# Kernel optimization log

Measured on AMD Instinct MI355X. Metric: run time of the kernel, lower is better.

## Reference

```python
import jax, jax.numpy as jnp
import numpy as np

N_NODES = 50000
N_EDGES = 800000
D_IN, D_HID, D_OUT = 128, 128, 64


def setup_inputs() -> dict:
    key = jax.random.key(0)
    ks = jax.random.split(key, 10)
    return {
        "x": jax.random.normal(ks[0], (N_NODES, D_IN), dtype=jnp.float32),
        "edge_row": jax.random.randint(ks[1], (N_EDGES,), 0, N_NODES, dtype=jnp.int32),
        "edge_col": jax.random.randint(ks[2], (N_EDGES,), 0, N_NODES, dtype=jnp.int32),
        "edge_val": jax.random.uniform(ks[3], (N_EDGES,), dtype=jnp.float32),
        "W1": jax.random.normal(ks[4], (D_IN, D_HID), dtype=jnp.float32) * (1.0 / np.sqrt(D_HID)),
        "b1": jax.random.normal(ks[5], (D_HID,), dtype=jnp.float32) * (1.0 / np.sqrt(D_HID)),
        "W2": jax.random.normal(ks[6], (D_HID, D_HID), dtype=jnp.float32) * (1.0 / np.sqrt(D_HID)),
        "b2": jax.random.normal(ks[7], (D_HID,), dtype=jnp.float32) * (1.0 / np.sqrt(D_HID)),
        "W3": jax.random.normal(ks[8], (D_HID, D_OUT), dtype=jnp.float32) * (1.0 / np.sqrt(D_OUT)),
        "b3": jax.random.normal(ks[9], (D_OUT,), dtype=jnp.float32) * (1.0 / np.sqrt(D_OUT)),
    }


def _gcn_layer(x, edge_row, edge_col, edge_val, W, b):
    # support = x @ W          : dense GEMM [N, d_out]
    support = x @ W
    # spmm(adj, support)[i] = sum_e with row[e]==i: val[e] * support[col[e]]
    gathered = support[edge_col] * edge_val[:, None]  # [E, d_out]
    agg = jax.ops.segment_sum(gathered, edge_row, num_segments=x.shape[0])
    return agg + b


def reference(x, edge_row, edge_col, edge_val, W1, b1, W2, b2, W3, b3):
    # Layer 1 + ReLU (dropout is identity in eval)
    h = jax.nn.relu(_gcn_layer(x, edge_row, edge_col, edge_val, W1, b1))
    # Layer 2 + ReLU
    h = jax.nn.relu(_gcn_layer(h, edge_row, edge_col, edge_val, W2, b2))
    # Layer 3 (no activation)
    return _gcn_layer(h, edge_row, edge_col, edge_val, W3, b3)
```

## Files before the change

### kernel.cpp

```cpp
#include <hip/hip_runtime.h>

#define N_NODES 50000
#define N_EDGES 800000
#define SCAN_TILE 2048
#define CNT_STRIDE 16
#define GEMM_BLOCKS 256

static_assert(N_NODES < 65536, "col must fit in 16 bits for packed CSR");

typedef __attribute__((ext_vector_type(4))) float f32x4;
typedef __attribute__((ext_vector_type(8))) short bf16x8;

__device__ inline unsigned short f32_to_bf16(float f) {
    unsigned int u = __builtin_bit_cast(unsigned int, f);
    u += 0x7FFF + ((u >> 16) & 1);
    return (unsigned short)(u >> 16);
}
__device__ inline float bf16_to_f32(unsigned short h) {
    unsigned int u = ((unsigned int)h) << 16;
    return __builtin_bit_cast(float, u);
}

#define W128  (128 * 128)
#define W64   (128 * 64)
#define CNT4  (N_NODES * CNT_STRIDE / 4)

__global__ void prep(const float* __restrict__ W1, const float* __restrict__ W2,
                     const float* __restrict__ W3, unsigned short* __restrict__ Wt1,
                     unsigned short* __restrict__ Wt2, unsigned short* __restrict__ Wt3,
                     int* __restrict__ cnt) {
    long long gid = (long long)blockIdx.x * blockDim.x + threadIdx.x;
    long long r = gid;
    if (r < W128) {
        int k = (int)r / 128, m = (int)r % 128;
        Wt1[m * 128 + k] = f32_to_bf16(W1[r]);
        return;
    }
    r -= W128;
    if (r < W128) {
        int k = (int)r / 128, m = (int)r % 128;
        Wt2[m * 128 + k] = f32_to_bf16(W2[r]);
        return;
    }
    r -= W128;
    if (r < W64) {
        int k = (int)r / 64, m = (int)r % 64;
        Wt3[m * 128 + k] = f32_to_bf16(W3[r]);
        return;
    }
    r -= W64;
    if (r < CNT4) {
        int4 z = {0, 0, 0, 0};
        reinterpret_cast<int4*>(cnt)[r] = z;
    }
}

__global__ void rank_histogram(const int* __restrict__ erow, int* __restrict__ cnt,
                               int* __restrict__ rank) {
    int e = blockIdx.x * blockDim.x + threadIdx.x;
    if (e < N_EDGES) rank[e] = atomicAdd(&cnt[(size_t)erow[e] * CNT_STRIDE], 1);
}

__global__ void scan_fused(const int* __restrict__ cnt, int* __restrict__ tsum,
                           int* __restrict__ done, int* __restrict__ rptr,
                           int n, int ntiles) {
    __shared__ int sums[256];
    __shared__ int off_s;
    const int t = threadIdx.x;
    const int b = blockIdx.x;
    const int base = b * SCAN_TILE + t * 8;
    int v[8], pref[8];
    int s = 0;
#pragma unroll
    for (int i = 0; i < 8; ++i) {
        v[i] = (base + i < n) ? cnt[(size_t)(base + i) * CNT_STRIDE] : 0;
        s += v[i];
    }
    sums[t] = s;
    __syncthreads();
    for (int off = 1; off < 256; off <<= 1) {
        int x = (t >= off) ? sums[t - off] : 0;
        __syncthreads();
        sums[t] += x;
        __syncthreads();
    }
    int run = sums[t] - s;
#pragma unroll
    for (int i = 0; i < 8; ++i) {
        pref[i] = run;
        run += v[i];
    }
    if (t == 255) {
        tsum[b] = run;
        __threadfence();
        atomicAdd(done, 1);
    }
    if (t == 0) {
        while (__hip_atomic_load(done, __ATOMIC_ACQUIRE, __HIP_MEMORY_SCOPE_AGENT) <
               ntiles) {
        }
        __threadfence();
        int off = 0;
        for (int i = 0; i < b; ++i) off += tsum[i];
        off_s = off;
        if (b == 0) {
            int tot = 0;
            for (int i = 0; i < ntiles; ++i) tot += tsum[i];
            rptr[n] = tot;
        }
    }
    __syncthreads();
    const int off = off_s;
#pragma unroll
    for (int i = 0; i < 8; ++i) {
        int idx = base + i;
        if (idx < n) rptr[idx] = pref[i] + off;
    }
}

template <int NOUT, bool OUT_BF16, bool IN_F32>
__device__ __forceinline__ void gemm_body(
    const void* __restrict__ Xin, const unsigned short* __restrict__ Wt,
    void* __restrict__ Yv, int N, int ntiles, int bid, int nblocks,
    unsigned short* Xs, unsigned short* Ws) {
    constexpr int K = 128;
    constexpr int KP = K + 8;
    constexpr int NT = NOUT / 16;

    const int tid = threadIdx.x;
    const int wave = tid >> 6;
    const int lane = tid & 63;
    const int m = lane & 15;
    const int quad = lane >> 4;
    const int rowbase = wave * 16;

    for (int idx = tid; idx < NOUT * 16; idx += 256) {
        int r = idx >> 4, ch = idx & 15;
        uint4 v = *reinterpret_cast<const uint4*>(Wt + r * K + ch * 8);
        *reinterpret_cast<uint4*>(Ws + r * KP + ch * 8) = v;
    }

    for (int tile = bid; tile < ntiles; tile += nblocks) {
        const int block_row = tile * 64;
        if (IN_F32) {
            const float* xf = (const float*)Xin;
            for (int idx = tid; idx < 64 * 16; idx += 256) {
                int r = idx >> 4, ch = idx & 15;
                int gr = block_row + r;
                if (gr >= N) gr = N - 1;
                const float4* xp =
                    reinterpret_cast<const float4*>(xf + (size_t)gr * K + ch * 8);
                float4 a = xp[0], b = xp[1];
                uint4 o;
                o.x = (unsigned int)f32_to_bf16(a.x) | ((unsigned int)f32_to_bf16(a.y) << 16);
                o.y = (unsigned int)f32_to_bf16(a.z) | ((unsigned int)f32_to_bf16(a.w) << 16);
                o.z = (unsigned int)f32_to_bf16(b.x) | ((unsigned int)f32_to_bf16(b.y) << 16);
                o.w = (unsigned int)f32_to_bf16(b.z) | ((unsigned int)f32_to_bf16(b.w) << 16);
                *reinterpret_cast<uint4*>(Xs + r * KP + ch * 8) = o;
            }
        } else {
            const unsigned short* xb = (const unsigned short*)Xin;
            for (int idx = tid; idx < 64 * 16; idx += 256) {
                int r = idx >> 4, ch = idx & 15;
                int gr = block_row + r;
                if (gr >= N) gr = N - 1;
                uint4 v = *reinterpret_cast<const uint4*>(xb + (size_t)gr * K + ch * 8);
                *reinterpret_cast<uint4*>(Xs + r * KP + ch * 8) = v;
            }
        }
        __syncthreads();

        f32x4 acc[NT];
#pragma unroll
        for (int t = 0; t < NT; ++t) acc[t] = (f32x4){0.f, 0.f, 0.f, 0.f};

#pragma unroll
        for (int kt = 0; kt < 4; ++kt) {
            bf16x8 a = *reinterpret_cast<const bf16x8*>(
                Xs + (rowbase + m) * KP + kt * 32 + quad * 8);
#pragma unroll
            for (int t = 0; t < NT; ++t) {
                bf16x8 b = *reinterpret_cast<const bf16x8*>(
                    Ws + (t * 16 + m) * KP + kt * 32 + quad * 8);
                acc[t] = __builtin_amdgcn_mfma_f32_16x16x32_bf16(a, b, acc[t], 0, 0, 0);
            }
        }
        __syncthreads();

#pragma unroll
        for (int t = 0; t < NT; ++t) {
#pragma unroll
            for (int r = 0; r < 4; ++r) {
                int grow = block_row + rowbase + quad * 4 + r;
                if (grow < N) {
                    if (OUT_BF16)
                        reinterpret_cast<unsigned short*>(Yv)[(size_t)grow * NOUT + t * 16 + m] =
                            f32_to_bf16(acc[t][r]);
                    else
                        reinterpret_cast<float*>(Yv)[(size_t)grow * NOUT + t * 16 + m] = acc[t][r];
                }
            }
        }
    }
}

template <int NOUT, bool OUT_BF16>
__global__ __launch_bounds__(256) void gemm_mfma(
    const unsigned short* __restrict__ Xb, const unsigned short* __restrict__ Wt,
    void* __restrict__ Yv, int N, int ntiles) {
    constexpr int KP = 128 + 8;
    __shared__ unsigned short Xs[64 * KP];
    __shared__ unsigned short Ws[NOUT * KP];
    gemm_body<NOUT, OUT_BF16, false>(Xb, Wt, Yv, N, ntiles, blockIdx.x, gridDim.x,
                                     Xs, Ws);
}

__global__ __launch_bounds__(256) void gemm1_fill(
    const float* __restrict__ x, const unsigned short* __restrict__ Wt,
    unsigned short* __restrict__ Yb, int N, int ntiles,
    const int* __restrict__ erow, const int* __restrict__ ecol,
    const float* __restrict__ eval, const int* __restrict__ rptr,
    const int* __restrict__ rank, unsigned int* __restrict__ cpack) {
    constexpr int KP = 128 + 8;
    __shared__ unsigned short Xs[64 * KP];
    __shared__ unsigned short Ws[128 * KP];
    if (blockIdx.x < GEMM_BLOCKS) {
        gemm_body<128, true, true>(x, Wt, Yb, N, ntiles, blockIdx.x, GEMM_BLOCKS,
                                   Xs, Ws);
    } else {
        int e = (blockIdx.x - GEMM_BLOCKS) * blockDim.x + threadIdx.x;
        if (e < N_EDGES) {
            int slot = rptr[erow[e]] + rank[e];
            unsigned int p = (unsigned int)(ecol[e] & 0xFFFF) |
                             ((unsigned int)f32_to_bf16(eval[e]) << 16);
            cpack[slot] = p;
        }
    }
}

__global__ void aggregate_bf16(const unsigned short* __restrict__ S,
                               const int* __restrict__ rptr,
                               const unsigned int* __restrict__ cpack,
                               const float* __restrict__ bias,
                               unsigned short* __restrict__ outb, int N) {
    const int node = blockIdx.x * (blockDim.x / 16) + threadIdx.x / 16;
    const int f8 = threadIdx.x & 15;
    if (node >= N) return;
    const int beg = rptr[node];
    const int end = rptr[node + 1];
    float acc[8];
#pragma unroll
    for (int i = 0; i < 8; ++i) acc[i] = bias[f8 * 8 + i];
    int j = beg;
    for (; j + 8 <= end; j += 8) {
        unsigned int p[8];
        uint4 s[8];
#pragma unroll
        for (int u = 0; u < 8; ++u) p[u] = cpack[j + u];
#pragma unroll
        for (int u = 0; u < 8; ++u)
            s[u] = *reinterpret_cast<const uint4*>(S + (size_t)(p[u] & 0xFFFF) * 128 + f8 * 8);
#pragma unroll
        for (int u = 0; u < 8; ++u) {
            const float v = bf16_to_f32((unsigned short)(p[u] >> 16));
            const unsigned short* sp = reinterpret_cast<const unsigned short*>(&s[u]);
#pragma unroll
            for (int i = 0; i < 8; ++i) acc[i] = fmaf(v, bf16_to_f32(sp[i]), acc[i]);
        }
    }
    if (j + 4 <= end) {
        unsigned int p[4];
        uint4 s[4];
#pragma unroll
        for (int u = 0; u < 4; ++u) p[u] = cpack[j + u];
#pragma unroll
        for (int u = 0; u < 4; ++u)
            s[u] = *reinterpret_cast<const uint4*>(S + (size_t)(p[u] & 0xFFFF) * 128 + f8 * 8);
#pragma unroll
        for (int u = 0; u < 4; ++u) {
            const float v = bf16_to_f32((unsigned short)(p[u] >> 16));
            const unsigned short* sp = reinterpret_cast<const unsigned short*>(&s[u]);
#pragma unroll
            for (int i = 0; i < 8; ++i) acc[i] = fmaf(v, bf16_to_f32(sp[i]), acc[i]);
        }
        j += 4;
    }
    if (j + 2 <= end) {
        unsigned int p[2];
        uint4 s[2];
#pragma unroll
        for (int u = 0; u < 2; ++u) p[u] = cpack[j + u];
#pragma unroll
        for (int u = 0; u < 2; ++u)
            s[u] = *reinterpret_cast<const uint4*>(S + (size_t)(p[u] & 0xFFFF) * 128 + f8 * 8);
#pragma unroll
        for (int u = 0; u < 2; ++u) {
            const float v = bf16_to_f32((unsigned short)(p[u] >> 16));
            const unsigned short* sp = reinterpret_cast<const unsigned short*>(&s[u]);
#pragma unroll
            for (int i = 0; i < 8; ++i) acc[i] = fmaf(v, bf16_to_f32(sp[i]), acc[i]);
        }
        j += 2;
    }
    if (j < end) {
        unsigned int p = cpack[j];
        uint4 s = *reinterpret_cast<const uint4*>(S + (size_t)(p & 0xFFFF) * 128 + f8 * 8);
        const float v = bf16_to_f32((unsigned short)(p >> 16));
        const unsigned short* sp = reinterpret_cast<const unsigned short*>(&s);
#pragma unroll
        for (int i = 0; i < 8; ++i) acc[i] = fmaf(v, bf16_to_f32(sp[i]), acc[i]);
    }
    unsigned short o[8];
#pragma unroll
    for (int i = 0; i < 8; ++i) o[i] = f32_to_bf16(fmaxf(acc[i], 0.0f));
    *reinterpret_cast<uint4*>(outb + (size_t)node * 128 + f8 * 8) =
        *reinterpret_cast<uint4*>(o);
}

__global__ void aggregate_bf16_64(const unsigned short* __restrict__ S,
                                  const int* __restrict__ rptr,
                                  const unsigned int* __restrict__ cpack,
                                  const float* __restrict__ bias,
                                  float* __restrict__ out, int N) {
    const int node = blockIdx.x * (blockDim.x / 16) + threadIdx.x / 16;
    const int f4 = threadIdx.x & 15;
    if (node >= N) return;
    const int beg = rptr[node];
    const int end = rptr[node + 1];
    float acc[4];
#pragma unroll
    for (int i = 0; i < 4; ++i) acc[i] = bias[f4 * 4 + i];
    int j = beg;
    for (; j + 8 <= end; j += 8) {
        unsigned int p[8];
        uint2 s[8];
#pragma unroll
        for (int u = 0; u < 8; ++u) p[u] = cpack[j + u];
#pragma unroll
        for (int u = 0; u < 8; ++u)
            s[u] = *reinterpret_cast<const uint2*>(S + (size_t)(p[u] & 0xFFFF) * 64 + f4 * 4);
#pragma unroll
        for (int u = 0; u < 8; ++u) {
            const float v = bf16_to_f32((unsigned short)(p[u] >> 16));
            const unsigned short* sp = reinterpret_cast<const unsigned short*>(&s[u]);
#pragma unroll
            for (int i = 0; i < 4; ++i) acc[i] = fmaf(v, bf16_to_f32(sp[i]), acc[i]);
        }
    }
    if (j + 4 <= end) {
        unsigned int p[4];
        uint2 s[4];
#pragma unroll
        for (int u = 0; u < 4; ++u) p[u] = cpack[j + u];
#pragma unroll
        for (int u = 0; u < 4; ++u)
            s[u] = *reinterpret_cast<const uint2*>(S + (size_t)(p[u] & 0xFFFF) * 64 + f4 * 4);
#pragma unroll
        for (int u = 0; u < 4; ++u) {
            const float v = bf16_to_f32((unsigned short)(p[u] >> 16));
            const unsigned short* sp = reinterpret_cast<const unsigned short*>(&s[u]);
#pragma unroll
            for (int i = 0; i < 4; ++i) acc[i] = fmaf(v, bf16_to_f32(sp[i]), acc[i]);
        }
        j += 4;
    }
    if (j + 2 <= end) {
        unsigned int p[2];
        uint2 s[2];
#pragma unroll
        for (int u = 0; u < 2; ++u) p[u] = cpack[j + u];
#pragma unroll
        for (int u = 0; u < 2; ++u)
            s[u] = *reinterpret_cast<const uint2*>(S + (size_t)(p[u] & 0xFFFF) * 64 + f4 * 4);
#pragma unroll
        for (int u = 0; u < 2; ++u) {
            const float v = bf16_to_f32((unsigned short)(p[u] >> 16));
            const unsigned short* sp = reinterpret_cast<const unsigned short*>(&s[u]);
#pragma unroll
            for (int i = 0; i < 4; ++i) acc[i] = fmaf(v, bf16_to_f32(sp[i]), acc[i]);
        }
        j += 2;
    }
    if (j < end) {
        unsigned int p = cpack[j];
        uint2 s = *reinterpret_cast<const uint2*>(S + (size_t)(p & 0xFFFF) * 64 + f4 * 4);
        const float v = bf16_to_f32((unsigned short)(p >> 16));
        const unsigned short* sp = reinterpret_cast<const unsigned short*>(&s);
#pragma unroll
        for (int i = 0; i < 4; ++i) acc[i] = fmaf(v, bf16_to_f32(sp[i]), acc[i]);
    }
    float4 o = {acc[0], acc[1], acc[2], acc[3]};
    *reinterpret_cast<float4*>(out + (size_t)node * 64 + f4 * 4) = o;
}

extern "C" void kernel_launch(void* const* d_in, const int* in_sizes, int n_in,
                              void* d_out, int out_size, void* d_ws, size_t ws_size,
                              hipStream_t stream) {
    const float* x    = (const float*)d_in[0];
    const int*   erow = (const int*)d_in[1];
    const int*   ecol = (const int*)d_in[2];
    const float* eval = (const float*)d_in[3];
    const float* W1   = (const float*)d_in[4];
    const float* b1   = (const float*)d_in[5];
    const float* W2   = (const float*)d_in[6];
    const float* b2   = (const float*)d_in[7];
    const float* W3   = (const float*)d_in[8];
    const float* b3   = (const float*)d_in[9];
    float* out = (float*)d_out;

    const size_t nf = (size_t)N_NODES * 128;
    unsigned short* Xb  = (unsigned short*)d_ws;
    unsigned short* Ab  = Xb + nf;
    unsigned short* Wt1 = Ab + nf;
    unsigned short* Wt2 = Wt1 + 128 * 128;
    unsigned short* Wt3 = Wt2 + 128 * 128;
    int*   cnt    = (int*)(Wt3 + 64 * 128);
    int*   rank   = cnt + (size_t)N_NODES * CNT_STRIDE;
    int*   rptr   = rank + N_EDGES;
    unsigned int* cpack = (unsigned int*)(rptr + N_NODES + 1);
    int*   stsum  = (int*)(cpack + N_EDGES);
    int*   done   = cnt + 1;

    const int blk = 256;
    const int ntiles_g = (N_NODES + 63) / 64;
    const int agg_grid = (int)(((long long)N_NODES * 16 + blk - 1) / blk);
    const int ntiles = (N_NODES + SCAN_TILE - 1) / SCAN_TILE;
    const int fill_blocks = (N_EDGES + blk - 1) / blk;

    {
        long long total = W128 + W128 + W64 + CNT4;
        prep<<<(int)((total + blk - 1) / blk), blk, 0, stream>>>(
            W1, W2, W3, Wt1, Wt2, Wt3, cnt);
    }
    rank_histogram<<<(N_EDGES + blk - 1) / blk, blk, 0, stream>>>(erow, cnt, rank);
    scan_fused<<<ntiles, 256, 0, stream>>>(cnt, stsum, done, rptr, N_NODES, ntiles);

    gemm1_fill<<<GEMM_BLOCKS + fill_blocks, 256, 0, stream>>>(
        x, Wt1, Ab, N_NODES, ntiles_g, erow, ecol, eval, rptr, rank, cpack);
    aggregate_bf16<<<agg_grid, blk, 0, stream>>>(Ab, rptr, cpack, b1, Xb, N_NODES);

    gemm_mfma<128, true><<<GEMM_BLOCKS, 256, 0, stream>>>(Xb, Wt2, Ab, N_NODES, ntiles_g);
    aggregate_bf16<<<agg_grid, blk, 0, stream>>>(Ab, rptr, cpack, b2, Xb, N_NODES);

    gemm_mfma<64, true><<<GEMM_BLOCKS, 256, 0, stream>>>(Xb, Wt3, Ab, N_NODES, ntiles_g);
    aggregate_bf16_64<<<agg_grid, blk, 0, stream>>>(Ab, rptr, cpack, b3, out, N_NODES);
}
```

Measured before the change: 262.8 us.

## Fuse sparse aggregation into following layer's MFMA GEMM via shared-memory tile

New measurement: 320.9 us. 22.1% more time.

```diff
diff --git a/kernel.cpp b/kernel.cpp
--- a/kernel.cpp
+++ b/kernel.cpp
@@ -5,6 +5,7 @@
 #define SCAN_TILE 2048
 #define CNT_STRIDE 16
 #define GEMM_BLOCKS 256
+#define HIST_BLOCKS ((N_EDGES + 255) / 256)
 
 static_assert(N_NODES < 65536, "col must fit in 16 bits for packed CSR");
 
@@ -25,12 +26,26 @@
 #define W64   (128 * 64)
 #define CNT4  (N_NODES * CNT_STRIDE / 4)
 
-__global__ void prep(const float* __restrict__ W1, const float* __restrict__ W2,
-                     const float* __restrict__ W3, unsigned short* __restrict__ Wt1,
-                     unsigned short* __restrict__ Wt2, unsigned short* __restrict__ Wt3,
-                     int* __restrict__ cnt) {
-    long long gid = (long long)blockIdx.x * blockDim.x + threadIdx.x;
-    long long r = gid;
+__global__ void zero_cnt(int* __restrict__ cnt) {
+    int i = blockIdx.x * blockDim.x + threadIdx.x;
+    if (i < CNT4) {
+        int4 z = {0, 0, 0, 0};
+        reinterpret_cast<int4*>(cnt)[i] = z;
+    }
+}
+
+__global__ void hist_wt(const int* __restrict__ erow, int* __restrict__ cnt,
+                        int* __restrict__ rank, const float* __restrict__ W1,
+                        const float* __restrict__ W2, const float* __restrict__ W3,
+                        unsigned short* __restrict__ Wt1,
+                        unsigned short* __restrict__ Wt2,
+                        unsigned short* __restrict__ Wt3) {
+    if (blockIdx.x < HIST_BLOCKS) {
+        int e = blockIdx.x * blockDim.x + threadIdx.x;
+        if (e < N_EDGES) rank[e] = atomicAdd(&cnt[(size_t)erow[e] * CNT_STRIDE], 1);
+        return;
+    }
+    long long r = (long long)(blockIdx.x - HIST_BLOCKS) * blockDim.x + threadIdx.x;
     if (r < W128) {
         int k = (int)r / 128, m = (int)r % 128;
         Wt1[m * 128 + k] = f32_to_bf16(W1[r]);
@@ -46,19 +61,7 @@
     if (r < W64) {
         int k = (int)r / 64, m = (int)r % 64;
         Wt3[m * 128 + k] = f32_to_bf16(W3[r]);
-        return;
-    }
-    r -= W64;
-    if (r < CNT4) {
-        int4 z = {0, 0, 0, 0};
-        reinterpret_cast<int4*>(cnt)[r] = z;
-    }
-}
-
-__global__ void rank_histogram(const int* __restrict__ erow, int* __restrict__ cnt,
-                               int* __restrict__ rank) {
-    int e = blockIdx.x * blockDim.x + threadIdx.x;
-    if (e < N_EDGES) rank[e] = atomicAdd(&cnt[(size_t)erow[e] * CNT_STRIDE], 1);
+    }
 }
 
 __global__ void scan_fused(const int* __restrict__ cnt, int* __restrict__ tsum,
@@ -118,15 +121,13 @@
     }
 }
 
-template <int NOUT, bool OUT_BF16, bool IN_F32>
-__device__ __forceinline__ void gemm_body(
-    const void* __restrict__ Xin, const unsigned short* __restrict__ Wt,
-    void* __restrict__ Yv, int N, int ntiles, int bid, int nblocks,
-    unsigned short* Xs, unsigned short* Ws) {
-    constexpr int K = 128;
-    constexpr int KP = K + 8;
+template <int NOUT>
+__device__ __forceinline__ void mfma_phase(const unsigned short* Xs,
+                                           const unsigned short* Ws,
+                                           unsigned short* __restrict__ Yb,
+                                           int block_row, int N) {
+    constexpr int KP = 128 + 8;
     constexpr int NT = NOUT / 16;
-
     const int tid = threadIdx.x;
     const int wave = tid >> 6;
     const int lane = tid & 63;
@@ -134,85 +135,31 @@
     const int quad = lane >> 4;
     const int rowbase = wave * 16;
 
-    for (int idx = tid; idx < NOUT * 16; idx += 256) {
-        int r = idx >> 4, ch = idx & 15;
-        uint4 v = *reinterpret_cast<const uint4*>(Wt + r * K + ch * 8);
-        *reinterpret_cast<uint4*>(Ws + r * KP + ch * 8) = v;
-    }
-
-    for (int tile = bid; tile < ntiles; tile += nblocks) {
-        const int block_row = tile * 64;
-        if (IN_F32) {
-            const float* xf = (const float*)Xin;
-            for (int idx = tid; idx < 64 * 16; idx += 256) {
-                int r = idx >> 4, ch = idx & 15;
-                int gr = block_row + r;
-                if (gr >= N) gr = N - 1;
-                const float4* xp =
-                    reinterpret_cast<const float4*>(xf + (size_t)gr * K + ch * 8);
-                float4 a = xp[0], b = xp[1];
-                uint4 o;
-                o.x = (unsigned int)f32_to_bf16(a.x) | ((unsigned int)f32_to_bf16(a.y) << 16);
-                o.y = (unsigned int)f32_to_bf16(a.z) | ((unsigned int)f32_to_bf16(a.w) << 16);
-                o.z = (unsigned int)f32_to_bf16(b.x) | ((unsigned int)f32_to_bf16(b.y) << 16);
-                o.w = (unsigned int)f32_to_bf16(b.z) | ((unsigned int)f32_to_bf16(b.w) << 16);
-                *reinterpret_cast<uint4*>(Xs + r * KP + ch * 8) = o;
-            }
-        } else {
-            const unsigned short* xb = (const unsigned short*)Xin;
-            for (int idx = tid; idx < 64 * 16; idx += 256) {
-                int r = idx >> 4, ch = idx & 15;
-                int gr = block_row + r;
-                if (gr >= N) gr = N - 1;
-                uint4 v = *reinterpret_cast<const uint4*>(xb + (size_t)gr * K + ch * 8);
-                *reinterpret_cast<uint4*>(Xs + r * KP + ch * 8) = v;
-            }
-        }
-        __syncthreads();
-
-        f32x4 acc[NT];
-#pragma unroll
-        for (int t = 0; t < NT; ++t) acc[t] = (f32x4){0.f, 0.f, 0.f, 0.f};
-
-#pragma unroll
-        for (int kt = 0; kt < 4; ++kt) {
-            bf16x8 a = *reinterpret_cast<const bf16x8*>(
-                Xs + (rowbase + m) * KP + kt * 32 + quad * 8);
-#pragma unroll
-            for (int t = 0; t < NT; ++t) {
-                bf16x8 b = *reinterpret_cast<const bf16x8*>(
-                    Ws + (t * 16 + m) * KP + kt * 32 + quad * 8);
-                acc[t] = __builtin_amdgcn_mfma_f32_16x16x32_bf16(a, b, acc[t], 0, 0, 0);
-            }
-        }
-        __syncthreads();
-
+    f32x4 acc[NT];
+#pragma unroll
+    for (int t = 0; t < NT; ++t) acc[t] = (f32x4){0.f, 0.f, 0.f, 0.f};
+
+#pragma unroll
+    for (int kt = 0; kt < 4; ++kt) {
+        bf16x8 a = *reinterpret_cast<const bf16x8*>(
+            Xs + (rowbase + m) * KP + kt * 32 + quad * 8);
 #pragma unroll
         for (int t = 0; t < NT; ++t) {
-#pragma unroll
-            for (int r = 0; r < 4; ++r) {
-                int grow = block_row + rowbase + quad * 4 + r;
-                if (grow < N) {
-                    if (OUT_BF16)
-                        reinterpret_cast<unsigned short*>(Yv)[(size_t)grow * NOUT + t * 16 + m] =
-                            f32_to_bf16(acc[t][r]);
-                    else
-                        reinterpret_cast<float*>(Yv)[(size_t)grow * NOUT + t * 16 + m] = acc[t][r];
-                }
-            }
-        }
-    }
-}
-
-template <int NOUT, bool OUT_BF16>
-__global__ __launch_bounds__(256) void gemm_mfma(
-    const unsigned short* __restrict__ Xb, const unsigned short* __restrict__ Wt,
-    void* __restrict__ Yv, int N, int ntiles) {
-    constexpr int KP = 128 + 8;
-    __shared__ unsigned short Xs[64 * KP];
-    __shared__ unsigned short Ws[NOUT * KP];
-    gemm_body<NOUT, OUT_BF16, false>(Xb, Wt, Yv, N, ntiles, blockIdx.x, gridDim.x,
-                                     Xs, Ws);
+            bf16x8 b = *reinterpret_cast<const bf16x8*>(
+                Ws + (t * 16 + m) * KP + kt * 32 + quad * 8);
+            acc[t] = __builtin_amdgcn_mfma_f32_16x16x32_bf16(a, b, acc[t], 0, 0, 0);
+        }
+    }
+
+#pragma unroll
+    for (int t = 0; t < NT; ++t) {
+#pragma unroll
+        for (int r = 0; r < 4; ++r) {
+            int grow = block_row + rowbase + quad * 4 + r;
+            if (grow < N)
+                Yb[(size_t)grow * NOUT + t * 16 + m] = f32_to_bf16(acc[t][r]);
+        }
+    }
 }
 
 __global__ __launch_bounds__(256) void gemm1_fill(
@@ -224,97 +171,171 @@
     constexpr int KP = 128 + 8;
     __shared__ unsigned short Xs[64 * KP];
     __shared__ unsigned short Ws[128 * KP];
-    if (blockIdx.x < GEMM_BLOCKS) {
-        gemm_body<128, true, true>(x, Wt, Yb, N, ntiles, blockIdx.x, GEMM_BLOCKS,
-                                   Xs, Ws);
-    } else {
-        int e = (blockIdx.x - GEMM_BLOCKS) * blockDim.x + threadIdx.x;
+    const int tid = threadIdx.x;
+
+    if (blockIdx.x >= GEMM_BLOCKS) {
+        int e = (blockIdx.x - GEMM_BLOCKS) * blockDim.x + tid;
         if (e < N_EDGES) {
             int slot = rptr[erow[e]] + rank[e];
             unsigned int p = (unsigned int)(ecol[e] & 0xFFFF) |
                              ((unsigned int)f32_to_bf16(eval[e]) << 16);
             cpack[slot] = p;
         }
-    }
-}
-
-__global__ void aggregate_bf16(const unsigned short* __restrict__ S,
-                               const int* __restrict__ rptr,
-                               const unsigned int* __restrict__ cpack,
-                               const float* __restrict__ bias,
-                               unsigned short* __restrict__ outb, int N) {
-    const int node = blockIdx.x * (blockDim.x / 16) + threadIdx.x / 16;
-    const int f8 = threadIdx.x & 15;
-    if (node >= N) return;
-    const int beg = rptr[node];
-    const int end = rptr[node + 1];
-    float acc[8];
-#pragma unroll
-    for (int i = 0; i < 8; ++i) acc[i] = bias[f8 * 8 + i];
-    int j = beg;
-    for (; j + 8 <= end; j += 8) {
-        unsigned int p[8];
-        uint4 s[8];
-#pragma unroll
-        for (int u = 0; u < 8; ++u) p[u] = cpack[j + u];
-#pragma unroll
-        for (int u = 0; u < 8; ++u)
-            s[u] = *reinterpret_cast<const uint4*>(S + (size_t)(p[u] & 0xFFFF) * 128 + f8 * 8);
-#pragma unroll
-        for (int u = 0; u < 8; ++u) {
-            const float v = bf16_to_f32((unsigned short)(p[u] >> 16));
-            const unsigned short* sp = reinterpret_cast<const unsigned short*>(&s[u]);
-#pragma unroll
-            for (int i = 0; i < 8; ++i) acc[i] = fmaf(v, bf16_to_f32(sp[i]), acc[i]);
-        }
-    }
-    if (j + 4 <= end) {
-        unsigned int p[4];
-        uint4 s[4];
-#pragma unroll
-        for (int u = 0; u < 4; ++u) p[u] = cpack[j + u];
-#pragma unroll
-        for (int u = 0; u < 4; ++u)
-            s[u] = *reinterpret_cast<const uint4*>(S + (size_t)(p[u] & 0xFFFF) * 128 + f8 * 8);
-#pragma unroll
-        for (int u = 0; u < 4; ++u) {
-            const float v = bf16_to_f32((unsigned short)(p[u] >> 16));
-            const unsigned short* sp = reinterpret_cast<const unsigned short*>(&s[u]);
-#pragma unroll
-            for (int i = 0; i < 8; ++i) acc[i] = fmaf(v, bf16_to_f32(sp[i]), acc[i]);
-        }
-        j += 4;
-    }
-    if (j + 2 <= end) {
-        unsigned int p[2];
-        uint4 s[2];
-#pragma unroll
-        for (int u = 0; u < 2; ++u) p[u] = cpack[j + u];
-#pragma unroll
-        for (int u = 0; u < 2; ++u)
-            s[u] = *reinterpret_cast<const uint4*>(S + (size_t)(p[u] & 0xFFFF) * 128 + f8 * 8);
-#pragma unroll
-        for (int u = 0; u < 2; ++u) {
-            const float v = bf16_to_f32((unsigned short)(p[u] >> 16));
-            const unsigned short* sp = reinterpret_cast<const unsigned short*>(&s[u]);
-#pragma unroll
-            for (int i = 0; i < 8; ++i) acc[i] = fmaf(v, bf16_to_f32(sp[i]), acc[i]);
-        }
-        j += 2;
-    }
-    if (j < end) {
-        unsigned int p = cpack[j];
-        uint4 s = *reinterpret_cast<const uint4*>(S + (size_t)(p & 0xFFFF) * 128 + f8 * 8);
-        const float v = bf16_to_f32((unsigned short)(p >> 16));
-        const unsigned short* sp = reinterpret_cast<const unsigned short*>(&s);
-#pragma unroll
-        for (int i = 0; i < 8; ++i) acc[i] = fmaf(v, bf16_to_f32(sp[i]), acc[i]);
-    }
-    unsigned short o[8];
-#pragma unroll
-    for (int i = 0; i < 8; ++i) o[i] = f32_to_bf16(fmaxf(acc[i], 0.0f));
-    *reinterpret_cast<uint4*>(outb + (size_t)node * 128 + f8 * 8) =
-        *reinterpret_cast<uint4*>(o);
+        return;
+    }
+
+    for (int idx = tid; idx < 128 * 16; idx += 256) {
+        int r = idx >> 4, ch = idx & 15;
+        uint4 v = *reinterpret_cast<const uint4*>(Wt + r * 128 + ch * 8);
+        *reinterpret_cast<uint4*>(Ws + r * KP + ch * 8) = v;
+    }
+
+    for (int tile = blockIdx.x; tile < ntiles; tile += GEMM_BLOCKS) {
+        const int block_row = tile * 64;
+        for (int idx = tid; idx < 64 * 16; idx += 256) {
+            int r = idx >> 4, ch = idx & 15;
+            int gr = block_row + r;
+            if (gr >= N) gr = N - 1;
+            const float4* xp =
+                reinterpret_cast<const float4*>(x + (size_t)gr * 128 + ch * 8);
+            float4 a = xp[0], b = xp[1];
+            uint4 o;
+            o.x = (unsigned int)f32_to_bf16(a.x) | ((unsigned int)f32_to_bf16(a.y) << 16);
+            o.y = (unsigned int)f32_to_bf16(a.z) | ((unsigned int)f32_to_bf16(a.w) << 16);
+            o.z = (unsigned int)f32_to_bf16(b.x) | ((unsigned int)f32_to_bf16(b.y) << 16);
+            o.w = (unsigned int)f32_to_bf16(b.z) | ((unsigned int)f32_to_bf16(b.w) << 16);
+            *reinterpret_cast<uint4*>(Xs + r * KP + ch * 8) = o;
+        }
+        __syncthreads();
+        mfma_phase<128>(Xs, Ws, Yb, block_row, N);
+        __syncthreads();
+    }
+}
+
+template <int NOUT>
+__global__ __launch_bounds__(256) void gemm_fused_agg(
+    const unsigned short* __restrict__ S,
+    const int* __restrict__ rptr, const unsigned int* __restrict__ cpack,
+    const float* __restrict__ bias,
+    const unsigned short* __restrict__ Wt,
+    unsigned short* __restrict__ Yb,
+    int N, int ntiles) {
+    constexpr int KP = 128 + 8;
+    __shared__ unsigned short Xs[64 * KP];
+    __shared__ unsigned short Ws[NOUT * KP];
+    const int tid = threadIdx.x;
+    const int group = tid >> 4;
+    const int f8 = tid & 15;
+
+    for (int idx = tid; idx < NOUT * 16; idx += 256) {
+        int r = idx >> 4, ch = idx & 15;
+        uint4 v = *reinterpret_cast<const uint4*>(Wt + r * 128 + ch * 8);
+        *reinterpret_cast<uint4*>(Ws + r * KP + ch * 8) = v;
+    }
+
+    float bv[8];
+#pragma unroll
+    for (int i = 0; i < 8; ++i) bv[i] = bias[f8 * 8 + i];
+
+    for (int tile = blockIdx.x; tile < ntiles; tile += gridDim.x) {
+        const int block_row = tile * 64;
+#pragma unroll
+        for (int r4 = 0; r4 < 4; ++r4) {
+            const int row = r4 * 16 + group;
+            const int node = block_row + row;
+            float acc[8];
+#pragma unroll
+            for (int i = 0; i < 8; ++i) acc[i] = bv[i];
+            if (node < N) {
+                const int beg = rptr[node];
+                const int end = rptr[node + 1];
+                int j = beg;
+                for (; j + 8 <= end; j += 8) {
+                    unsigned int p[8];
+                    uint4 s[8];
+#pragma unroll
+                    for (int u = 0; u < 8; ++u) p[u] = cpack[j + u];
+#pragma unroll
+                    for (int u = 0; u < 8; ++u)
+                        s[u] = *reinterpret_cast<const uint4*>(
+                            S + (size_t)(p[u] & 0xFFFF) * 128 + f8 * 8);
+#pragma unroll
+                    for (int u = 0; u < 8; ++u) {
+                        const float v = bf16_to_f32((unsigned short)(p[u] >> 16));
+                        const unsigned short* sp =
+                            reinterpret_cast<const unsigned short*>(&s[u]);
+#pragma unroll
+                        for (int i = 0; i < 8; ++i)
+                            acc[i] = fmaf(v, bf16_to_f32(sp[i]), acc[i]);
+                    }
+                }
+                if (j + 4 <= end) {
+                    unsigned int p[4];
+                    uint4 s[4];
+#pragma unroll
+                    for (int u = 0; u < 4; ++u) p[u] = cpack[j + u];
+#pragma unroll
+                    for (int u = 0; u < 4; ++u)
+                        s[u] = *reinterpret_cast<const uint4*>(
+                            S + (size_t)(p[u] & 0xFFFF) * 128 + f8 * 8);
+#pragma unroll
+                    for (int u = 0; u < 4; ++u) {
+                        const float v = bf16_to_f32((unsigned short)(p[u] >> 16));
+                        const unsigned short* sp =
+                            reinterpret_cast<const unsigned short*>(&s[u]);
+#pragma unroll
+                        for (int i = 0; i < 8; ++i)
+                            acc[i] = fmaf(v, bf16_to_f32(sp[i]), acc[i]);
+                    }
+                    j += 4;
+                }
+                if (j + 2 <= end) {
+                    unsigned int p[2];
+                    uint4 s[2];
+#pragma unroll
+                    for (int u = 0; u < 2; ++u) p[u] = cpack[j + u];
+#pragma unroll
+                    for (int u = 0; u < 2; ++u)
+                        s[u] = *reinterpret_cast<const uint4*>(
+                            S + (size_t)(p[u] & 0xFFFF) * 128 + f8 * 8);
+#pragma unroll
+                    for (int u = 0; u < 2; ++u) {
+                        const float v = bf16_to_f32((unsigned short)(p[u] >> 16));
+                        const unsigned short* sp =
+                            reinterpret_cast<const unsigned short*>(&s[u]);
+#pragma unroll
+                        for (int i = 0; i < 8; ++i)
+                            acc[i] = fmaf(v, bf16_to_f32(sp[i]), acc[i]);
+                    }
+                    j += 2;
+                }
+                if (j < end) {
+                    unsigned int p = cpack[j];
+                    uint4 s = *reinterpret_cast<const uint4*>(
+                        S + (size_t)(p & 0xFFFF) * 128 + f8 * 8);
+                    const float v = bf16_to_f32((unsigned short)(p >> 16));
+                    const unsigned short* sp =
+                        reinterpret_cast<const unsigned short*>(&s);
+#pragma unroll
+                    for (int i = 0; i < 8; ++i)
+                        acc[i] = fmaf(v, bf16_to_f32(sp[i]), acc[i]);
+                }
+            }
+            uint4 o;
+            o.x = (unsigned int)f32_to_bf16(fmaxf(acc[0], 0.f)) |
+                  ((unsigned int)f32_to_bf16(fmaxf(acc[1], 0.f)) << 16);
+            o.y = (unsigned int)f32_to_bf16(fmaxf(acc[2], 0.f)) |
+                  ((unsigned int)f32_to_bf16(fmaxf(acc[3], 0.f)) << 16);
+            o.z = (unsigned int)f32_to_bf16(fmaxf(acc[4], 0.f)) |
+                  ((unsigned int)f32_to_bf16(fmaxf(acc[5], 0.f)) << 16);
+            o.w = (unsigned int)f32_to_bf16(fmaxf(acc[6], 0.f)) |
+                  ((unsigned int)f32_to_bf16(fmaxf(acc[7], 0.f)) << 16);
+            *reinterpret_cast<uint4*>(Xs + row * KP + f8 * 8) = o;
+        }
+        __syncthreads();
+        mfma_phase<NOUT>(Xs, Ws, Yb, block_row, N);
+        __syncthreads();
+    }
 }
 
 __global__ void aggregate_bf16_64(const unsigned short* __restrict__ S,
@@ -409,9 +430,9 @@
     float* out = (float*)d_out;
 
     const size_t nf = (size_t)N_NODES * 128;
-    unsigned short* Xb  = (unsigned short*)d_ws;
-    unsigned short* Ab  = Xb + nf;
-    unsigned short* Wt1 = Ab + nf;
+    unsigned short* SA  = (unsigned short*)d_ws;
+    unsigned short* SB  = SA + nf;
+    unsigned short* Wt1 = SB + nf;
     unsigned short* Wt2 = Wt1 + 128 * 128;
     unsigned short* Wt3 = Wt2 + 128 * 128;
     int*   cnt    = (int*)(Wt3 + 64 * 128);
@@ -425,23 +446,21 @@
     const int ntiles_g = (N_NODES + 63) / 64;
     const int agg_grid = (int)(((long long)N_NODES * 16 + blk - 1) / blk);
     const int ntiles = (N_NODES + SCAN_TILE - 1) / SCAN_TILE;
-    const int fill_blocks = (N_EDGES + blk - 1) / blk;
-
-    {
-        long long total = W128 + W128 + W64 + CNT4;
-        prep<<<(int)((total + blk - 1) / blk), blk, 0, stream>>>(
-            W1, W2, W3, Wt1, Wt2, Wt3, cnt);
-    }
-    rank_histogram<<<(N_EDGES + blk - 1) / blk, blk, 0, stream>>>(erow, cnt, rank);
+    const int wt_blocks = (W128 + W128 + W64 + blk - 1) / blk;
+
+    zero_cnt<<<(CNT4 + blk - 1) / blk, blk, 0, stream>>>(cnt);
+    hist_wt<<<HIST_BLOCKS + wt_blocks, blk, 0, stream>>>(erow, cnt, rank, W1, W2, W3,
+                                                         Wt1, Wt2, Wt3);
     scan_fused<<<ntiles, 256, 0, stream>>>(cnt, stsum, done, rptr, N_NODES, ntiles);
 
-    gemm1_fill<<<GEMM_BLOCKS + fill_blocks, 256, 0, stream>>>(
-        x, Wt1, Ab, N_NODES, ntiles_g, erow, ecol, eval, rptr, rank, cpack);
-    aggregate_bf16<<<agg_grid, blk, 0, stream>>>(Ab, rptr, cpack, b1, Xb, N_NODES);
-
-    gemm_mfma<128, true><<<GEMM_BLOCKS, 256, 0, stream>>>(Xb, Wt2, Ab, N_NODES, ntiles_g);
-    aggregate_bf16<<<agg_grid, blk, 0, stream>>>(Ab, rptr, cpack, b2, Xb, N_NODES);
-
-    gemm_mfma<64, true><<<GEMM_BLOCKS, 256, 0, stream>>>(Xb, Wt3, Ab, N_NODES, ntiles_g);
-    aggregate_bf16_64<<<agg_grid, blk, 0, stream>>>(Ab, rptr, cpack, b3, out, N_NODES);
-}
+    gemm1_fill<<<GEMM_BLOCKS + HIST_BLOCKS, 256, 0, stream>>>(
+        x, Wt1, SA, N_NODES, ntiles_g, erow, ecol, eval, rptr, rank, cpack);
+
+    gemm_fused_agg<128><<<GEMM_BLOCKS, 256, 0, stream>>>(
+        SA, rptr, cpack, b1, Wt2, SB, N_NODES, ntiles_g);
+
+    gemm_fused_agg<64><<<GEMM_BLOCKS, 256, 0, stream>>>(
+        SB, rptr, cpack, b2, Wt3, SA, N_NODES, ntiles_g);
+
+    aggregate_bf16_64<<<agg_grid, blk, 0, stream>>>(SA, rptr, cpack, b3, out, N_NODES);
+}
```
